# Performance work log

Hardware: AMD Instinct MI355X
Metric: run time of the kernel (lower is better)

## Reference

```python
import jax, jax.numpy as jnp
import numpy as np
from jax import lax

B, CIN, COUT, H, W, DG, K = 4, 128, 64, 128, 128, 16, 9
MAX_RES = 10.0  # max_residue_magnitude


def conv3x3(x, w, b):
    y = lax.conv_general_dilated(x, w, (1, 1), [(1, 1), (1, 1)],
                                 dimension_numbers=('NCHW', 'OIHW', 'NCHW'))
    return y + b[None, :, None, None]


def setup_inputs() -> dict:
    key = jax.random.key(0)
    ks = jax.random.split(key, 8)
    def rn(k, shape, s=0.05):
        return jax.random.normal(k, shape, jnp.float32) * s
    return {
        "x": jax.random.normal(ks[0], (B, CIN, H, W), jnp.float32),
        "extra_feat": jax.random.normal(ks[1], (B, 3 * COUT, H, W), jnp.float32),
        "w1": rn(ks[2], (COUT, 3 * COUT, 3, 3)), "b1": jnp.zeros((COUT,), jnp.float32),
        "w2": rn(ks[3], (COUT, COUT, 3, 3)), "b2": jnp.zeros((COUT,), jnp.float32),
        "w3": rn(ks[4], (COUT, COUT, 3, 3)), "b3": jnp.zeros((COUT,), jnp.float32),
        "w4": rn(ks[5], (27 * DG, COUT, 3, 3), 0.02), "b4": jnp.zeros((27 * DG,), jnp.float32),
        "weight": rn(ks[6], (COUT, CIN, 3, 3)), "bias": jnp.zeros((COUT,), jnp.float32),
    }


def deform_conv2d(x, offset, mask, weight, bias):
    # Modulated deformable conv, torchvision layout:
    # offset: [B, 2*DG*K, H, W] ordered (group, kernel_pos, (dy,dx))
    # mask:   [B, DG*K, H, W]
    Bn, Cin, Hh, Ww = x.shape
    Cg = Cin // DG
    off = offset.reshape(Bn, DG, K, 2, Hh, Ww)
    dy, dx = off[:, :, :, 0], off[:, :, :, 1]
    m = mask.reshape(Bn, DG, K, Hh, Ww)
    ki = (jnp.arange(K) // 3).reshape(1, 1, K, 1, 1).astype(x.dtype)
    kj = (jnp.arange(K) % 3).reshape(1, 1, K, 1, 1).astype(x.dtype)
    hh = jnp.arange(Hh, dtype=x.dtype).reshape(1, 1, 1, Hh, 1)
    ww = jnp.arange(Ww, dtype=x.dtype).reshape(1, 1, 1, 1, Ww)
    # sampling positions (stride=1, padding=1, dilation=1)
    py = hh - 1.0 + ki + dy  # [B,DG,K,H,W]
    px = ww - 1.0 + kj + dx
    y0 = jnp.floor(py)
    x0 = jnp.floor(px)
    ly = py - y0
    lx = px - x0
    xf = x.reshape(Bn, DG, Cg, Hh * Ww)

    def gather(yi, xi, wgt):
        valid = (yi >= 0) & (yi < Hh) & (xi >= 0) & (xi < Ww)
        yc = jnp.clip(yi, 0, Hh - 1).astype(jnp.int32)
        xc = jnp.clip(xi, 0, Ww - 1).astype(jnp.int32)
        idx = (yc * Ww + xc).reshape(Bn, DG, 1, K * Hh * Ww)
        g = jnp.take_along_axis(xf, jnp.broadcast_to(idx, (Bn, DG, Cg, K * Hh * Ww)), axis=3)
        g = g.reshape(Bn, DG, Cg, K, Hh, Ww)
        w_ = (wgt * valid.astype(x.dtype))[:, :, None]  # [B,DG,1,K,H,W]
        return g * w_

    val = (gather(y0, x0, (1 - ly) * (1 - lx))
           + gather(y0, x0 + 1, (1 - ly) * lx)
           + gather(y0 + 1, x0, ly * (1 - lx))
           + gather(y0 + 1, x0 + 1, ly * lx))
    val = val * m[:, :, None]  # modulation
    wk = weight.reshape(weight.shape[0], DG, Cg, K)
    out = jnp.einsum('bgckhw,ogck->bohw', val, wk) + bias[None, :, None, None]
    return out


def reference(x, extra_feat, w1, b1, w2, b2, w3, b3, w4, b4, weight, bias):
    lrelu = lambda t: jax.nn.leaky_relu(t, 0.1)
    t = lrelu(conv3x3(extra_feat, w1, b1))
    t = lrelu(conv3x3(t, w2, b2))
    t = lrelu(conv3x3(t, w3, b3))
    out = conv3x3(t, w4, b4)
    o1, o2, m = jnp.split(out, 3, axis=1)
    offset = MAX_RES * jnp.tanh(jnp.concatenate([o1, o2], axis=1))
    mask = jax.nn.sigmoid(m)
    return deform_conv2d(x, offset, mask, weight, bias)
```

## Files before the change

kernel.cpp:

```cpp
#include <hip/hip_runtime.h>
#include <cstdint>

#define H_ 128
#define W_ 128
#define HW 16384

typedef _Float16 f16x8 __attribute__((ext_vector_type(8)));
typedef _Float16 f16x4 __attribute__((ext_vector_type(4)));
typedef _Float16 f16x2 __attribute__((ext_vector_type(2)));
typedef float f32x4 __attribute__((ext_vector_type(4)));

__global__ __launch_bounds__(256)
void prep_all(const float* __restrict__ wd, const float* __restrict__ w1,
              const float* __restrict__ w2, const float* __restrict__ w3,
              const float* __restrict__ w4, const float* __restrict__ x,
              const float* __restrict__ ef,
              _Float16* __restrict__ wp, _Float16* __restrict__ A1,
              _Float16* __restrict__ A2, _Float16* __restrict__ A3,
              _Float16* __restrict__ A4, _Float16* __restrict__ xt,
              _Float16* __restrict__ ef_t) {
    __shared__ __align__(16) _Float16 t[128 * 200];
    const int bx  = blockIdx.x;
    const int tid = threadIdx.x;
    if (bx < 384) {
        int i = bx * 256 + tid;
        int kc = i % 96;
        int go = i / 96;
        int o = go & 63, g = go >> 6;
        float v = 0.f;
        if (kc < 72) { int k = kc >> 3, c = kc & 7; v = wd[(o * 128 + g * 8 + c) * 9 + k]; }
        wp[i] = (_Float16)v;
    } else if (bx < 2256) {
        const float* w; _Float16* Ap; int CIN, COUT, COpad, base;
        if (bx < 816)       { w = w1; Ap = A1; CIN = 192; COUT = 64;  COpad = 64;  base = 384; }
        else if (bx < 960)  { w = w2; Ap = A2; CIN = 64;  COUT = 64;  COpad = 64;  base = 816; }
        else if (bx < 1104) { w = w3; Ap = A3; CIN = 64;  COUT = 64;  COpad = 64;  base = 960; }
        else                { w = w4; Ap = A4; CIN = 64;  COUT = 432; COpad = 512; base = 1104; }
        int i = (bx - base) * 256 + tid;
        int kb = i / (COpad * 8);
        int rem = i - kb * (COpad * 8);
        int co = rem >> 3, j = rem & 7;
        int k = kb * 8 + j;
        int s = k / CIN;
        int ci = k - s * CIN;
        int kh = s / 3, kw = s % 3;
        float v = (co < COUT) ? w[((size_t)co * CIN + ci) * 9 + kh * 3 + kw] : 0.f;
        Ap[i] = (_Float16)v;
    } else if (bx < 6352) {
        int i = (bx - 2256) * 256 + tid;
        int px = i & 16383;
        int g  = (i >> 14) & 15;
        int b  = i >> 18;
        const float* xp = x + ((size_t)(b * 128 + g * 8) * HW) + px;
        f16x8 v;
        #pragma unroll
        for (int c = 0; c < 8; ++c) v[c] = (_Float16)xp[c * HW];
        *(f16x8*)(xt + (size_t)i * 8) = v;
    } else {
        int bb = bx - 6352;
        int b = bb >> 7, h = bb & 127;
        for (int i = tid; i < 192 * 128; i += 256) {
            int c = i >> 7, w = i & 127;
            t[w * 200 + c] = (_Float16)ef[((size_t)(b * 192 + c) * 128 + h) * 128 + w];
        }
        __syncthreads();
        _Float16* ob = ef_t + ((size_t)(b * 128 + h) * 128) * 192;
        for (int i = tid; i < 128 * 24; i += 256) {
            int px = i / 24, c8 = i % 24;
            *(f16x8*)(ob + px * 192 + c8 * 8) = *(const f16x8*)(t + px * 200 + c8 * 8);
        }
    }
}

template<int CIN_T, int COUT_T, int COpad_T, int NWM, int NWN, int MT, int NT,
         int ACT, int MINW>
__global__ __launch_bounds__(256, MINW)
void conv_mfma2(const _Float16* __restrict__ in, const _Float16* __restrict__ Ap,
                const float* __restrict__ bias, void* __restrict__ outp,
                _Float16* __restrict__ mskp) {
    constexpr int PX = 64;
    static_assert(NWM * NWN == 4 && NWN * NT * 16 == PX, "tiling");
    constexpr int TW  = PX + 2;
    constexpr int CPC = CIN_T / 8;
    constexpr int NKH = (CIN_T == 64) ? 3 : 1;
    constexpr int NST = 3 / NKH;
    constexpr int TC  = NKH * TW * CPC;
    constexpr int COg = NWM * MT * 16;
    __shared__ __align__(16) _Float16 lds[TC * 8];

    const int tid  = threadIdx.x;
    const int bxr  = (blockIdx.x & 7) * 128 + (blockIdx.x >> 3);
    const int ns   = bxr & 1;
    const int bh   = bxr >> 1;
    const int b    = bh >> 7;
    const int h    = bh & 127;
    const int cogB = blockIdx.y * COg;
    const int wv   = tid >> 6;
    const int wv_m = wv / NWN;
    const int wv_n = wv - wv_m * NWN;
    const int lane = tid & 63;
    const int quad = lane >> 4;
    const int l16  = lane & 15;
    const int w0g  = ns * PX;

    f32x4 acc[MT][NT];
    #pragma unroll
    for (int mt = 0; mt < MT; ++mt)
        #pragma unroll
        for (int nt = 0; nt < NT; ++nt) acc[mt][nt] = (f32x4){0.f, 0.f, 0.f, 0.f};

    const _Float16* inb = in + (size_t)b * (HW * CIN_T);

    auto stage = [&](int s) {
        for (int i = tid; i < TC; i += 256) {
            int kh_l = i / (TW * CPC);
            int r2   = i - kh_l * (TW * CPC);
            int wp_  = r2 / CPC;
            int c8   = r2 - wp_ * CPC;
            int kh   = s * NKH + kh_l;
            int hh   = h - 1 + kh;
            int w    = w0g + wp_ - 1;
            f16x8 v = (f16x8){0, 0, 0, 0, 0, 0, 0, 0};
            if ((unsigned)hh < 128u && (unsigned)w < 128u)
                v = *(const f16x8*)(inb + (hh * 128 + w) * CIN_T + c8 * 8);
            int slot = (c8 & ~7) | ((c8 & 7) ^ (wp_ & 7));
            ((f16x8*)lds)[(kh_l * TW + wp_) * CPC + slot] = v;
        }
    };

    auto compute = [&](int s) {
        #pragma unroll
        for (int kh_l = 0; kh_l < NKH; ++kh_l) {
            const int kh = s * NKH + kh_l;
            #pragma unroll
            for (int kwi = 0; kwi < 3; ++kwi) {
                #pragma unroll
                for (int ci32 = 0; ci32 < CIN_T / 32; ++ci32) {
                    const int kb0 = (kh * 3 + kwi) * CPC + ci32 * 4;
                    f16x8 aF[MT];
                    #pragma unroll
                    for (int mt = 0; mt < MT; ++mt) {
                        int co_m = cogB + (wv_m * MT + mt) * 16 + l16;
                        aF[mt] = *(const f16x8*)(Ap + ((size_t)(kb0 + quad) * COpad_T + co_m) * 8);
                    }
                    const int c8v = ci32 * 4 + quad;
                    #pragma unroll
                    for (int nt = 0; nt < NT; ++nt) {
                        int n  = (wv_n * NT + nt) * 16 + l16;
                        int wq = n + kwi;
                        int slot = (c8v & ~7) | ((c8v & 7) ^ (wq & 7));
                        f16x8 bF = ((const f16x8*)lds)[(kh_l * TW + wq) * CPC + slot];
                        #pragma unroll
                        for (int mt = 0; mt < MT; ++mt)
                            acc[mt][nt] = __builtin_amdgcn_mfma_f32_16x16x32_f16(aF[mt], bF, acc[mt][nt], 0, 0, 0);
                    }
                }
            }
        }
    };

    #pragma unroll 1
    for (int s = 0; s < NST; ++s) {
        __syncthreads();
        stage(s);
        __syncthreads();
        compute(s);
    }

    if constexpr (ACT == 1) {
        _Float16* ob = (_Float16*)outp + ((size_t)((b * 128 + h) * 128) + w0g) * 64;
        #pragma unroll
        for (int mt = 0; mt < MT; ++mt) {
            int co_b = (wv_m * MT + mt) * 16 + quad * 4;
            #pragma unroll
            for (int nt = 0; nt < NT; ++nt) {
                int px = (wv_n * NT + nt) * 16 + l16;
                f16x4 sv;
                #pragma unroll
                for (int r = 0; r < 4; ++r) {
                    float v = acc[mt][nt][r] + bias[co_b + r];
                    v = v > 0.f ? v : 0.1f * v;
                    sv[r] = (_Float16)v;
                }
                *(f16x4*)(ob + px * 64 + co_b) = sv;
            }
        }
    } else {
        _Float16* off2 = (_Float16*)outp;
        const int pxbase = h * 128 + w0g;
        #pragma unroll
        for (int mt = 0; mt < MT; ++mt) {
            int co_base = cogB + (wv_m * MT + mt) * 16 + quad * 4;
            #pragma unroll
            for (int r2 = 0; r2 < 2; ++r2) {
                int co0 = co_base + 2 * r2;
                if (co0 < 288) {
                    int g = co0 / 18;
                    int k = (co0 - g * 18) >> 1;
                    float bv0 = bias[co0], bv1 = bias[co0 + 1];
                    #pragma unroll
                    for (int nt = 0; nt < NT; ++nt) {
                        int px = (wv_n * NT + nt) * 16 + l16;
                        float v0 = acc[mt][nt][2 * r2]     + bv0;
                        float v1 = acc[mt][nt][2 * r2 + 1] + bv1;
                        float e0 = __expf(2.f * v0);
                        float e1 = __expf(2.f * v1);
                        f16x2 ov;
                        ov[0] = (_Float16)(10.f * (1.f - 2.f / (e0 + 1.f)));
                        ov[1] = (_Float16)(10.f * (1.f - 2.f / (e1 + 1.f)));
                        *(f16x2*)(off2 + (((size_t)(b * 16 + g) * 9 + k) * HW + pxbase + px) * 2) = ov;
                    }
                } else if (co0 < 432) {
                    #pragma unroll
                    for (int j = 0; j < 2; ++j) {
                        int co = co0 + j;
                        int mm = co - 288;
                        int g = mm / 9;
                        int k = mm - g * 9;
                        float bv = bias[co];
                        #pragma unroll
                        for (int nt = 0; nt < NT; ++nt) {
                            int px = (wv_n * NT + nt) * 16 + l16;
                            float v = acc[mt][nt][2 * r2 + j] + bv;
                            v = 1.f / (1.f + __expf(-v));
                            mskp[((size_t)(b * 16 + g) * 9 + k) * HW + pxbase + px] = (_Float16)v;
                        }
                    }
                }
            }
        }
    }
}

__global__ __launch_bounds__(256, 4)
void deform_fused(const _Float16* __restrict__ xt, const _Float16* __restrict__ off2,
                  const _Float16* __restrict__ msk, const _Float16* __restrict__ wp,
                  const float* __restrict__ bias, float* __restrict__ out) {
    __shared__ __align__(16) char vlds[2 * 64 * 256];
    const int tid  = threadIdx.x;
    const int bx   = (blockIdx.x & 7) * 128 + (blockIdx.x >> 3);
    const int ns   = bx & 1;
    const int bh   = bx >> 1;
    const int b    = bh >> 7;
    const int hrow = bh & 127;
    const int wv   = tid >> 6;
    const int lane = tid & 63;
    const int quad = lane >> 4;
    const int l16  = lane & 15;

    const int pxl   = tid & 63;
    const int kq    = tid >> 6;
    const int wglob = ns * 64 + pxl;
    const int pxg   = hrow * 128 + wglob;

    {
        f32x4 z = (f32x4){0.f, 0.f, 0.f, 0.f};
        for (int i = tid; i < 2048; i += 256) ((f32x4*)vlds)[i] = z;
    }
    __syncthreads();

    const _Float16* o2b = off2 + (size_t)b * 16 * 9 * HW * 2;
    const _Float16* mb  = msk  + (size_t)b * 16 * 9 * HW;

    f32x4 acc[4];
    #pragma unroll
    for (int nt = 0; nt < 4; ++nt) acc[nt] = (f32x4){0.f, 0.f, 0.f, 0.f};

    f16x2 od_c[3]; _Float16 m_c[3];
    #pragma unroll
    for (int i = 0; i < 3; ++i) {
        int k = kq + 4 * i;
        if (k < 9) {
            od_c[i] = *(const f16x2*)(o2b + ((size_t)(0 * 9 + k) * HW + pxg) * 2);
            m_c[i]  = mb[(size_t)(0 * 9 + k) * HW + pxg];
        }
    }

    #pragma unroll 1
    for (int gl = 0; gl < 16; ++gl) {
        const _Float16* xg = xt + ((size_t)(b * 16 + gl) * HW) * 8;
        char* vb = vlds + (gl & 1) * 16384;

        f16x8 aF[3];
        const _Float16* wg = wp + ((size_t)(gl * 64 + wv * 16 + l16)) * 96 + quad * 8;
        #pragma unroll
        for (int s = 0; s < 3; ++s) aF[s] = *(const f16x8*)(wg + s * 32);

        f16x2 od_n[3]; _Float16 m_n[3];
        if (gl < 15) {
            #pragma unroll
            for (int i = 0; i < 3; ++i) {
                int k = kq + 4 * i;
                if (k < 9) {
                    od_n[i] = *(const f16x2*)(o2b + ((size_t)((gl + 1) * 9 + k) * HW + pxg) * 2);
                    m_n[i]  = mb[(size_t)((gl + 1) * 9 + k) * HW + pxg];
                }
            }
        }

        #pragma unroll
        for (int i = 0; i < 3; ++i) {
            int k = kq + 4 * i;
            if (k < 9) {
                float dy = (float)od_c[i][0];
                float dx = (float)od_c[i][1];
                float m  = (float)m_c[i];
                float py  = (float)(hrow - 1 + k / 3) + dy;
                float pxf = (float)(wglob - 1 + k % 3) + dx;
                float y0f = floorf(py), x0f = floorf(pxf);
                float ly = py - y0f, lx = pxf - x0f;
                int y0 = (int)y0f, x0 = (int)x0f;
                int y1 = y0 + 1,  x1 = x0 + 1;
                float vy0 = ((unsigned)y0 < 128u) ? 1.f : 0.f;
                float vy1 = ((unsigned)y1 < 128u) ? 1.f : 0.f;
                float vx0 = ((unsigned)x0 < 128u) ? 1.f : 0.f;
                float vx1 = ((unsigned)x1 < 128u) ? 1.f : 0.f;
                float w00 = (1.f - ly) * (1.f - lx) * vy0 * vx0 * m;
                float w01 = (1.f - ly) * lx         * vy0 * vx1 * m;
                float w10 = ly * (1.f - lx)         * vy1 * vx0 * m;
                float w11 = ly * lx                 * vy1 * vx1 * m;
                int yc0 = min(max(y0, 0), 127), yc1 = min(max(y1, 0), 127);
                int xc0 = min(max(x0, 0), 127), xc1 = min(max(x1, 0), 127);
                f16x8 c00 = *(const f16x8*)(xg + (yc0 * W_ + xc0) * 8);
                f16x8 c01 = *(const f16x8*)(xg + (yc0 * W_ + xc1) * 8);
                f16x8 c10 = *(const f16x8*)(xg + (yc1 * W_ + xc0) * 8);
                f16x8 c11 = *(const f16x8*)(xg + (yc1 * W_ + xc1) * 8);
                _Float16 h00 = (_Float16)w00, h01 = (_Float16)w01;
                _Float16 h10 = (_Float16)w10, h11 = (_Float16)w11;
                f16x8 vv = c00 * h00 + c01 * h01 + c10 * h10 + c11 * h11;
                int chunk = k ^ (pxl & 15);
                *(f16x8*)(vb + pxl * 256 + chunk * 16) = vv;
            }
        }
        __syncthreads();

        #pragma unroll
        for (int nt = 0; nt < 4; ++nt) {
            int row = nt * 16 + l16;
            int sw  = row & 15;
            #pragma unroll
            for (int s = 0; s < 3; ++s) {
                f16x8 bF = *(const f16x8*)(vb + row * 256 + (((s << 2) + quad) ^ sw) * 16);
                acc[nt] = __builtin_amdgcn_mfma_f32_16x16x32_f16(aF[s], bF, acc[nt], 0, 0, 0);
            }
        }

        #pragma unroll
        for (int i = 0; i < 3; ++i) { od_c[i] = od_n[i]; m_c[i] = m_n[i]; }
    }

    __syncthreads();
    float* vf = (float*)vlds;
    #pragma unroll
    for (int r = 0; r < 4; ++r) {
        int o = wv * 16 + quad * 4 + r;
        #pragma unroll
        for (int nt = 0; nt < 4; ++nt) {
            int col = nt ^ quad;
            vf[o * 64 + col * 16 + l16] = acc[nt][r];
        }
    }
    __syncthreads();
    float* ob = out + ((size_t)(b * 64)) * HW + hrow * 128 + ns * 64;
    #pragma unroll
    for (int it = 0; it < 4; ++it) {
        int slot = tid + it * 256;
        int o    = slot >> 4;
        int p4   = slot & 15;
        int col  = (p4 >> 2) ^ ((o >> 2) & 3);
        f32x4 v = *(const f32x4*)(vf + o * 64 + col * 16 + (p4 & 3) * 4);
        float bv = bias[o];
        float4 sv = make_float4(v[0] + bv, v[1] + bv, v[2] + bv, v[3] + bv);
        *(float4*)(ob + (size_t)o * HW + p4 * 4) = sv;
    }
}

extern "C" void kernel_launch(void* const* d_in, const int* in_sizes, int n_in,
                              void* d_out, int out_size, void* d_ws, size_t ws_size,
                              hipStream_t stream) {
    const float* x  = (const float*)d_in[0];
    const float* ef = (const float*)d_in[1];
    const float* w1 = (const float*)d_in[2];
    const float* b1 = (const float*)d_in[3];
    const float* w2 = (const float*)d_in[4];
    const float* b2 = (const float*)d_in[5];
    const float* w3 = (const float*)d_in[6];
    const float* b3 = (const float*)d_in[7];
    const float* w4 = (const float*)d_in[8];
    const float* b4 = (const float*)d_in[9];
    const float* wd = (const float*)d_in[10];
    const float* bd = (const float*)d_in[11];
    float* out = (float*)d_out;

    char* ws = (char*)d_ws;
    _Float16* ef_t = (_Float16*)(ws);
    _Float16* tA   = (_Float16*)(ws + 25165824);
    _Float16* tB   = (_Float16*)(ws + 33554432);
    _Float16* off2 = (_Float16*)(ws + 41943040);
    _Float16* mskb = (_Float16*)(ws + 79691776);
    _Float16* wpd  = (_Float16*)(ws + 98566144);
    _Float16* A1   = (_Float16*)(ws + 98762752);
    _Float16* A2   = (_Float16*)(ws + 98983936);
    _Float16* A3   = (_Float16*)(ws + 99057664);
    _Float16* A4   = (_Float16*)(ws + 99131392);
    _Float16* xtb  = (_Float16*)(ws + 99721216);

    prep_all<<<6864, 256, 0, stream>>>(wd, w1, w2, w3, w4, x, ef,
                                       wpd, A1, A2, A3, A4, xtb, ef_t);

    conv_mfma2<192,  64,  64,  2,  2, 2, 2, 1, 4><<<dim3(1024, 1), 256, 0, stream>>>(ef_t, A1, b1, tA, nullptr);
    conv_mfma2< 64,  64,  64,  2,  2, 2, 2, 1, 4><<<dim3(1024, 1), 256, 0, stream>>>(tA, A2, b2, tB, nullptr);
    conv_mfma2< 64,  64,  64,  2,  2, 2, 2, 1, 4><<<dim3(1024, 1), 256, 0, stream>>>(tB, A3, b3, tA, nullptr);
    conv_mfma2< 64, 432, 512,  2,  2, 4, 2, 2, 2><<<dim3(1024, 4), 256, 0, stream>>>(tA, A4, b4, off2, mskb);

    deform_fused<<<1024, 256, 0, stream>>>(xtb, off2, mskb, wpd, bd, out);
}
```

Before: 315.0 us.

## Halve deform tile width to 32 pixels and double block count

```diff
diff --git a/kernel.cpp b/kernel.cpp
--- a/kernel.cpp
+++ b/kernel.cpp
@@ -236,11 +236,11 @@
 void deform_fused(const _Float16* __restrict__ xt, const _Float16* __restrict__ off2,
                   const _Float16* __restrict__ msk, const _Float16* __restrict__ wp,
                   const float* __restrict__ bias, float* __restrict__ out) {
-    __shared__ __align__(16) char vlds[2 * 64 * 256];
+    __shared__ __align__(16) char vlds[2 * 32 * 256];
     const int tid  = threadIdx.x;
-    const int bx   = (blockIdx.x & 7) * 128 + (blockIdx.x >> 3);
-    const int ns   = bx & 1;
-    const int bh   = bx >> 1;
+    const int bx   = (blockIdx.x & 7) * 256 + (blockIdx.x >> 3);
+    const int nq   = bx & 3;
+    const int bh   = bx >> 2;
     const int b    = bh >> 7;
     const int hrow = bh & 127;
     const int wv   = tid >> 6;
@@ -248,60 +248,59 @@
     const int quad = lane >> 4;
     const int l16  = lane & 15;
 
-    const int pxl   = tid & 63;
-    const int kq    = tid >> 6;
-    const int wglob = ns * 64 + pxl;
+    const int pxl   = tid & 31;
+    const int slot  = tid >> 5;
+    const int wglob = nq * 32 + pxl;
     const int pxg   = hrow * 128 + wglob;
+    const bool has2 = (slot == 0);
 
     {
         f32x4 z = (f32x4){0.f, 0.f, 0.f, 0.f};
-        for (int i = tid; i < 2048; i += 256) ((f32x4*)vlds)[i] = z;
+        for (int i = tid; i < 1024; i += 256) ((f32x4*)vlds)[i] = z;
     }
     __syncthreads();
 
     const _Float16* o2b = off2 + (size_t)b * 16 * 9 * HW * 2;
     const _Float16* mb  = msk  + (size_t)b * 16 * 9 * HW;
 
-    f32x4 acc[4];
-    #pragma unroll
-    for (int nt = 0; nt < 4; ++nt) acc[nt] = (f32x4){0.f, 0.f, 0.f, 0.f};
-
-    f16x2 od_c[3]; _Float16 m_c[3];
-    #pragma unroll
-    for (int i = 0; i < 3; ++i) {
-        int k = kq + 4 * i;
-        if (k < 9) {
-            od_c[i] = *(const f16x2*)(o2b + ((size_t)(0 * 9 + k) * HW + pxg) * 2);
-            m_c[i]  = mb[(size_t)(0 * 9 + k) * HW + pxg];
-        }
+    f32x4 acc[2];
+    acc[0] = (f32x4){0.f, 0.f, 0.f, 0.f};
+    acc[1] = (f32x4){0.f, 0.f, 0.f, 0.f};
+
+    f16x2 od_c[2]; _Float16 m_c[2];
+    od_c[0] = *(const f16x2*)(o2b + ((size_t)slot * HW + pxg) * 2);
+    m_c[0]  = mb[(size_t)slot * HW + pxg];
+    od_c[1] = od_c[0]; m_c[1] = m_c[0];
+    if (has2) {
+        od_c[1] = *(const f16x2*)(o2b + ((size_t)8 * HW + pxg) * 2);
+        m_c[1]  = mb[(size_t)8 * HW + pxg];
     }
 
     #pragma unroll 1
     for (int gl = 0; gl < 16; ++gl) {
         const _Float16* xg = xt + ((size_t)(b * 16 + gl) * HW) * 8;
-        char* vb = vlds + (gl & 1) * 16384;
+        char* vb = vlds + (gl & 1) * 8192;
 
         f16x8 aF[3];
         const _Float16* wg = wp + ((size_t)(gl * 64 + wv * 16 + l16)) * 96 + quad * 8;
         #pragma unroll
         for (int s = 0; s < 3; ++s) aF[s] = *(const f16x8*)(wg + s * 32);
 
-        f16x2 od_n[3]; _Float16 m_n[3];
+        f16x2 od_n[2]; _Float16 m_n[2];
+        od_n[0] = od_c[0]; od_n[1] = od_c[1]; m_n[0] = m_c[0]; m_n[1] = m_c[1];
         if (gl < 15) {
-            #pragma unroll
-            for (int i = 0; i < 3; ++i) {
-                int k = kq + 4 * i;
-                if (k < 9) {
-                    od_n[i] = *(const f16x2*)(o2b + ((size_t)((gl + 1) * 9 + k) * HW + pxg) * 2);
-                    m_n[i]  = mb[(size_t)((gl + 1) * 9 + k) * HW + pxg];
-                }
-            }
-        }
-
-        #pragma unroll
-        for (int i = 0; i < 3; ++i) {
-            int k = kq + 4 * i;
-            if (k < 9) {
+            od_n[0] = *(const f16x2*)(o2b + ((size_t)((gl + 1) * 9 + slot) * HW + pxg) * 2);
+            m_n[0]  = mb[(size_t)((gl + 1) * 9 + slot) * HW + pxg];
+            if (has2) {
+                od_n[1] = *(const f16x2*)(o2b + ((size_t)((gl + 1) * 9 + 8) * HW + pxg) * 2);
+                m_n[1]  = mb[(size_t)((gl + 1) * 9 + 8) * HW + pxg];
+            }
+        }
+
+        #pragma unroll
+        for (int i = 0; i < 2; ++i) {
+            if (i == 0 || has2) {
+                int k = (i == 0) ? slot : 8;
                 float dy = (float)od_c[i][0];
                 float dx = (float)od_c[i][1];
                 float m  = (float)m_c[i];
@@ -335,7 +334,7 @@
         __syncthreads();
 
         #pragma unroll
-        for (int nt = 0; nt < 4; ++nt) {
+        for (int nt = 0; nt < 2; ++nt) {
             int row = nt * 16 + l16;
             int sw  = row & 15;
             #pragma unroll
@@ -345,8 +344,7 @@
             }
         }
 
-        #pragma unroll
-        for (int i = 0; i < 3; ++i) { od_c[i] = od_n[i]; m_c[i] = m_n[i]; }
+        od_c[0] = od_n[0]; od_c[1] = od_n[1]; m_c[0] = m_n[0]; m_c[1] = m_n[1];
     }
 
     __syncthreads();
@@ -355,20 +353,20 @@
     for (int r = 0; r < 4; ++r) {
         int o = wv * 16 + quad * 4 + r;
         #pragma unroll
-        for (int nt = 0; nt < 4; ++nt) {
-            int col = nt ^ quad;
-            vf[o * 64 + col * 16 + l16] = acc[nt][r];
+        for (int nt = 0; nt < 2; ++nt) {
+            int col = nt ^ (quad & 1);
+            vf[o * 32 + col * 16 + l16] = acc[nt][r];
         }
     }
     __syncthreads();
-    float* ob = out + ((size_t)(b * 64)) * HW + hrow * 128 + ns * 64;
+    float* ob = out + ((size_t)(b * 64)) * HW + hrow * 128 + nq * 32;
     #pragma unroll
-    for (int it = 0; it < 4; ++it) {
-        int slot = tid + it * 256;
-        int o    = slot >> 4;
-        int p4   = slot & 15;
-        int col  = (p4 >> 2) ^ ((o >> 2) & 3);
-        f32x4 v = *(const f32x4*)(vf + o * 64 + col * 16 + (p4 & 3) * 4);
+    for (int it = 0; it < 2; ++it) {
+        int sl  = tid + it * 256;
+        int o   = sl >> 3;
+        int p4  = sl & 7;
+        int col = (p4 >> 2) ^ ((o >> 2) & 1);
+        f32x4 v = *(const f32x4*)(vf + o * 32 + col * 16 + (p4 & 3) * 4);
         float bv = bias[o];
         float4 sv = make_float4(v[0] + bv, v[1] + bv, v[2] + bv, v[3] + bv);
         *(float4*)(ob + (size_t)o * HW + p4 * 4) = sv;
@@ -413,5 +411,5 @@
     conv_mfma2< 64,  64,  64,  2,  2, 2, 2, 1, 4><<<dim3(1024, 1), 256, 0, stream>>>(tB, A3, b3, tA, nullptr);
     conv_mfma2< 64, 432, 512,  2,  2, 4, 2, 2, 2><<<dim3(1024, 4), 256, 0, stream>>>(tA, A4, b4, off2, mskb);
 
-    deform_fused<<<1024, 256, 0, stream>>>(xtb, off2, mskb, wpd, bd, out);
+    deform_fused<<<2048, 256, 0, stream>>>(xtb, off2, mskb, wpd, bd, out);
 }
```

Result: slower. 323.6 us (+2.7%).

## Software-pipeline deformable gathers one group ahead of MFMA compute

Applied to the files above, without the earlier changes.

```diff
diff --git a/kernel.cpp b/kernel.cpp
--- a/kernel.cpp
+++ b/kernel.cpp
@@ -266,45 +266,22 @@
     #pragma unroll
     for (int nt = 0; nt < 4; ++nt) acc[nt] = (f32x4){0.f, 0.f, 0.f, 0.f};
 
-    f16x2 od_c[3]; _Float16 m_c[3];
+    int ch[3];
     #pragma unroll
-    for (int i = 0; i < 3; ++i) {
-        int k = kq + 4 * i;
-        if (k < 9) {
-            od_c[i] = *(const f16x2*)(o2b + ((size_t)(0 * 9 + k) * HW + pxg) * 2);
-            m_c[i]  = mb[(size_t)(0 * 9 + k) * HW + pxg];
-        }
-    }
-
-    #pragma unroll 1
-    for (int gl = 0; gl < 16; ++gl) {
+    for (int i = 0; i < 3; ++i) ch[i] = (((kq + 4 * i) ^ (pxl & 15)) << 4);
+
+    f16x8 g00[3], g01[3], g10[3], g11[3];
+    _Float16 h00[3], h01[3], h10[3], h11[3];
+
+    auto issue = [&](int gl, const f16x2* od, const _Float16* m) {
         const _Float16* xg = xt + ((size_t)(b * 16 + gl) * HW) * 8;
-        char* vb = vlds + (gl & 1) * 16384;
-
-        f16x8 aF[3];
-        const _Float16* wg = wp + ((size_t)(gl * 64 + wv * 16 + l16)) * 96 + quad * 8;
-        #pragma unroll
-        for (int s = 0; s < 3; ++s) aF[s] = *(const f16x8*)(wg + s * 32);
-
-        f16x2 od_n[3]; _Float16 m_n[3];
-        if (gl < 15) {
-            #pragma unroll
-            for (int i = 0; i < 3; ++i) {
-                int k = kq + 4 * i;
-                if (k < 9) {
-                    od_n[i] = *(const f16x2*)(o2b + ((size_t)((gl + 1) * 9 + k) * HW + pxg) * 2);
-                    m_n[i]  = mb[(size_t)((gl + 1) * 9 + k) * HW + pxg];
-                }
-            }
-        }
-
         #pragma unroll
         for (int i = 0; i < 3; ++i) {
             int k = kq + 4 * i;
             if (k < 9) {
-                float dy = (float)od_c[i][0];
-                float dx = (float)od_c[i][1];
-                float m  = (float)m_c[i];
+                float dy = (float)od[i][0];
+                float dx = (float)od[i][1];
+                float mm = (float)m[i];
                 float py  = (float)(hrow - 1 + k / 3) + dy;
                 float pxf = (float)(wglob - 1 + k % 3) + dx;
                 float y0f = floorf(py), x0f = floorf(pxf);
@@ -315,25 +292,74 @@
                 float vy1 = ((unsigned)y1 < 128u) ? 1.f : 0.f;
                 float vx0 = ((unsigned)x0 < 128u) ? 1.f : 0.f;
                 float vx1 = ((unsigned)x1 < 128u) ? 1.f : 0.f;
-                float w00 = (1.f - ly) * (1.f - lx) * vy0 * vx0 * m;
-                float w01 = (1.f - ly) * lx         * vy0 * vx1 * m;
-                float w10 = ly * (1.f - lx)         * vy1 * vx0 * m;
-                float w11 = ly * lx                 * vy1 * vx1 * m;
+                h00[i] = (_Float16)((1.f - ly) * (1.f - lx) * vy0 * vx0 * mm);
+                h01[i] = (_Float16)((1.f - ly) * lx         * vy0 * vx1 * mm);
+                h10[i] = (_Float16)(ly * (1.f - lx)         * vy1 * vx0 * mm);
+                h11[i] = (_Float16)(ly * lx                 * vy1 * vx1 * mm);
                 int yc0 = min(max(y0, 0), 127), yc1 = min(max(y1, 0), 127);
                 int xc0 = min(max(x0, 0), 127), xc1 = min(max(x1, 0), 127);
-                f16x8 c00 = *(const f16x8*)(xg + (yc0 * W_ + xc0) * 8);
-                f16x8 c01 = *(const f16x8*)(xg + (yc0 * W_ + xc1) * 8);
-                f16x8 c10 = *(const f16x8*)(xg + (yc1 * W_ + xc0) * 8);
-                f16x8 c11 = *(const f16x8*)(xg + (yc1 * W_ + xc1) * 8);
-                _Float16 h00 = (_Float16)w00, h01 = (_Float16)w01;
-                _Float16 h10 = (_Float16)w10, h11 = (_Float16)w11;
-                f16x8 vv = c00 * h00 + c01 * h01 + c10 * h10 + c11 * h11;
-                int chunk = k ^ (pxl & 15);
-                *(f16x8*)(vb + pxl * 256 + chunk * 16) = vv;
-            }
-        }
+                g00[i] = *(const f16x8*)(xg + (yc0 * W_ + xc0) * 8);
+                g01[i] = *(const f16x8*)(xg + (yc0 * W_ + xc1) * 8);
+                g10[i] = *(const f16x8*)(xg + (yc1 * W_ + xc0) * 8);
+                g11[i] = *(const f16x8*)(xg + (yc1 * W_ + xc1) * 8);
+            }
+        }
+    };
+
+    auto finish = [&](int gl) {
+        char* vb = vlds + (gl & 1) * 16384;
+        #pragma unroll
+        for (int i = 0; i < 3; ++i) {
+            int k = kq + 4 * i;
+            if (k < 9) {
+                f16x8 vv = g00[i] * h00[i] + g01[i] * h01[i]
+                         + g10[i] * h10[i] + g11[i] * h11[i];
+                *(f16x8*)(vb + pxl * 256 + ch[i]) = vv;
+            }
+        }
+    };
+
+    {
+        f16x2 od0[3]; _Float16 m0[3];
+        #pragma unroll
+        for (int i = 0; i < 3; ++i) {
+            od0[i] = (f16x2){0, 0}; m0[i] = (_Float16)0.f;
+            int k = kq + 4 * i;
+            if (k < 9) {
+                od0[i] = *(const f16x2*)(o2b + ((size_t)k * HW + pxg) * 2);
+                m0[i]  = mb[(size_t)k * HW + pxg];
+            }
+        }
+        issue(0, od0, m0);
+    }
+
+    #pragma unroll 1
+    for (int gl = 0; gl < 16; ++gl) {
+        f16x2 od_n[3]; _Float16 m_n[3];
+        #pragma unroll
+        for (int i = 0; i < 3; ++i) { od_n[i] = (f16x2){0, 0}; m_n[i] = (_Float16)0.f; }
+        if (gl < 15) {
+            #pragma unroll
+            for (int i = 0; i < 3; ++i) {
+                int k = kq + 4 * i;
+                if (k < 9) {
+                    od_n[i] = *(const f16x2*)(o2b + ((size_t)((gl + 1) * 9 + k) * HW + pxg) * 2);
+                    m_n[i]  = mb[(size_t)((gl + 1) * 9 + k) * HW + pxg];
+                }
+            }
+        }
+
+        f16x8 aF[3];
+        const _Float16* wg = wp + ((size_t)(gl * 64 + wv * 16 + l16)) * 96 + quad * 8;
+        #pragma unroll
+        for (int s = 0; s < 3; ++s) aF[s] = *(const f16x8*)(wg + s * 32);
+
+        finish(gl);
         __syncthreads();
 
+        if (gl < 15) issue(gl + 1, od_n, m_n);
+
+        char* vb = vlds + (gl & 1) * 16384;
         #pragma unroll
         for (int nt = 0; nt < 4; ++nt) {
             int row = nt * 16 + l16;
@@ -344,9 +370,6 @@
                 acc[nt] = __builtin_amdgcn_mfma_f32_16x16x32_f16(aF[s], bF, acc[nt], 0, 0, 0);
             }
         }
-
-        #pragma unroll
-        for (int i = 0; i < 3; ++i) { od_c[i] = od_n[i]; m_c[i] = m_n[i]; }
     }
 
     __syncthreads();
```

New measurement: 316.7 us. About the same (+0.5%).

## Stage per-group input window in LDS for deformable bilinear gathers

Applied to the files above, without the earlier changes.

```diff
diff --git a/kernel.cpp b/kernel.cpp
--- a/kernel.cpp
+++ b/kernel.cpp
@@ -24,11 +24,17 @@
     const int tid = threadIdx.x;
     if (bx < 384) {
         int i = bx * 256 + tid;
-        int kc = i % 96;
-        int go = i / 96;
-        int o = go & 63, g = go >> 6;
+        int e = i & 7;
+        int chunk = i >> 3;
+        int o = chunk & 63;
+        int tq = chunk >> 6;
+        int q = tq & 3;
+        int u = tq >> 2;
+        int s = u % 3;
+        int g = u / 3;
+        int k = s * 4 + q;
         float v = 0.f;
-        if (kc < 72) { int k = kc >> 3, c = kc & 7; v = wd[(o * 128 + g * 8 + c) * 9 + k]; }
+        if (k < 9) v = wd[(o * 128 + g * 8 + e) * 9 + k];
         wp[i] = (_Float16)v;
     } else if (bx < 2256) {
         const float* w; _Float16* Ap; int CIN, COUT, COpad, base;
@@ -232,11 +238,15 @@
     }
 }
 
-__global__ __launch_bounds__(256, 4)
+__global__ __launch_bounds__(256, 3)
 void deform_fused(const _Float16* __restrict__ xt, const _Float16* __restrict__ off2,
                   const _Float16* __restrict__ msk, const _Float16* __restrict__ wp,
                   const float* __restrict__ bias, float* __restrict__ out) {
-    __shared__ __align__(16) char vlds[2 * 64 * 256];
+    constexpr int WROW = 24, WCOL = 89;
+    __shared__ __align__(16) char lds_all[WROW * WCOL * 16 + 64 * 256];
+    char* winb = lds_all;
+    char* vb   = lds_all + WROW * WCOL * 16;
+
     const int tid  = threadIdx.x;
     const int bx   = (blockIdx.x & 7) * 128 + (blockIdx.x >> 3);
     const int ns   = bx & 1;
@@ -252,12 +262,13 @@
     const int kq    = tid >> 6;
     const int wglob = ns * 64 + pxl;
     const int pxg   = hrow * 128 + wglob;
+    const int rbase = hrow - 11;
+    const int cbase = ns * 64 - 11;
 
     {
         f32x4 z = (f32x4){0.f, 0.f, 0.f, 0.f};
-        for (int i = tid; i < 2048; i += 256) ((f32x4*)vlds)[i] = z;
-    }
-    __syncthreads();
+        for (int i = tid; i < 1024; i += 256) ((f32x4*)vb)[i] = z;
+    }
 
     const _Float16* o2b = off2 + (size_t)b * 16 * 9 * HW * 2;
     const _Float16* mb  = msk  + (size_t)b * 16 * 9 * HW;
@@ -266,45 +277,29 @@
     #pragma unroll
     for (int nt = 0; nt < 4; ++nt) acc[nt] = (f32x4){0.f, 0.f, 0.f, 0.f};
 
-    f16x2 od_c[3]; _Float16 m_c[3];
-    #pragma unroll
-    for (int i = 0; i < 3; ++i) {
-        int k = kq + 4 * i;
-        if (k < 9) {
-            od_c[i] = *(const f16x2*)(o2b + ((size_t)(0 * 9 + k) * HW + pxg) * 2);
-            m_c[i]  = mb[(size_t)(0 * 9 + k) * HW + pxg];
-        }
-    }
-
-    #pragma unroll 1
-    for (int gl = 0; gl < 16; ++gl) {
+    auto stage_win = [&](int gl) {
         const _Float16* xg = xt + ((size_t)(b * 16 + gl) * HW) * 8;
-        char* vb = vlds + (gl & 1) * 16384;
-
-        f16x8 aF[3];
-        const _Float16* wg = wp + ((size_t)(gl * 64 + wv * 16 + l16)) * 96 + quad * 8;
-        #pragma unroll
-        for (int s = 0; s < 3; ++s) aF[s] = *(const f16x8*)(wg + s * 32);
-
-        f16x2 od_n[3]; _Float16 m_n[3];
-        if (gl < 15) {
-            #pragma unroll
-            for (int i = 0; i < 3; ++i) {
-                int k = kq + 4 * i;
-                if (k < 9) {
-                    od_n[i] = *(const f16x2*)(o2b + ((size_t)((gl + 1) * 9 + k) * HW + pxg) * 2);
-                    m_n[i]  = mb[(size_t)((gl + 1) * 9 + k) * HW + pxg];
-                }
-            }
-        }
-
+        #pragma unroll
+        for (int it = 0; it < 9; ++it) {
+            int i = tid + it * 256;
+            if (i < WROW * WCOL) {
+                int r = i / WCOL;
+                int c = i - r * WCOL;
+                int ry = min(max(rbase + r, 0), 127);
+                int cx = min(max(cbase + c, 0), 127);
+                *(f16x8*)(winb + i * 16) = *(const f16x8*)(xg + (ry * 128 + cx) * 8);
+            }
+        }
+    };
+
+    auto gather = [&](const f16x2* od, const _Float16* m) {
         #pragma unroll
         for (int i = 0; i < 3; ++i) {
             int k = kq + 4 * i;
             if (k < 9) {
-                float dy = (float)od_c[i][0];
-                float dx = (float)od_c[i][1];
-                float m  = (float)m_c[i];
+                float dy = (float)od[i][0];
+                float dx = (float)od[i][1];
+                float mm = (float)m[i];
                 float py  = (float)(hrow - 1 + k / 3) + dy;
                 float pxf = (float)(wglob - 1 + k % 3) + dx;
                 float y0f = floorf(py), x0f = floorf(pxf);
@@ -315,24 +310,59 @@
                 float vy1 = ((unsigned)y1 < 128u) ? 1.f : 0.f;
                 float vx0 = ((unsigned)x0 < 128u) ? 1.f : 0.f;
                 float vx1 = ((unsigned)x1 < 128u) ? 1.f : 0.f;
-                float w00 = (1.f - ly) * (1.f - lx) * vy0 * vx0 * m;
-                float w01 = (1.f - ly) * lx         * vy0 * vx1 * m;
-                float w10 = ly * (1.f - lx)         * vy1 * vx0 * m;
-                float w11 = ly * lx                 * vy1 * vx1 * m;
-                int yc0 = min(max(y0, 0), 127), yc1 = min(max(y1, 0), 127);
-                int xc0 = min(max(x0, 0), 127), xc1 = min(max(x1, 0), 127);
-                f16x8 c00 = *(const f16x8*)(xg + (yc0 * W_ + xc0) * 8);
-                f16x8 c01 = *(const f16x8*)(xg + (yc0 * W_ + xc1) * 8);
-                f16x8 c10 = *(const f16x8*)(xg + (yc1 * W_ + xc0) * 8);
-                f16x8 c11 = *(const f16x8*)(xg + (yc1 * W_ + xc1) * 8);
-                _Float16 h00 = (_Float16)w00, h01 = (_Float16)w01;
-                _Float16 h10 = (_Float16)w10, h11 = (_Float16)w11;
+                _Float16 h00 = (_Float16)((1.f - ly) * (1.f - lx) * vy0 * vx0 * mm);
+                _Float16 h01 = (_Float16)((1.f - ly) * lx         * vy0 * vx1 * mm);
+                _Float16 h10 = (_Float16)(ly * (1.f - lx)         * vy1 * vx0 * mm);
+                _Float16 h11 = (_Float16)(ly * lx                 * vy1 * vx1 * mm);
+                int ci = (y0 - rbase) * WCOL + (x0 - cbase);
+                f16x8 c00 = *(const f16x8*)(winb + ci * 16);
+                f16x8 c01 = *(const f16x8*)(winb + ci * 16 + 16);
+                f16x8 c10 = *(const f16x8*)(winb + (ci + WCOL) * 16);
+                f16x8 c11 = *(const f16x8*)(winb + (ci + WCOL) * 16 + 16);
                 f16x8 vv = c00 * h00 + c01 * h01 + c10 * h10 + c11 * h11;
-                int chunk = k ^ (pxl & 15);
-                *(f16x8*)(vb + pxl * 256 + chunk * 16) = vv;
-            }
-        }
+                *(f16x8*)(vb + pxl * 256 + ((k ^ (pxl & 15)) << 4)) = vv;
+            }
+        }
+    };
+
+    f16x2 od_c[3]; _Float16 m_c[3];
+    #pragma unroll
+    for (int i = 0; i < 3; ++i) {
+        od_c[i] = (f16x2){0, 0}; m_c[i] = (_Float16)0.f;
+        int k = kq + 4 * i;
+        if (k < 9) {
+            od_c[i] = *(const f16x2*)(o2b + ((size_t)k * HW + pxg) * 2);
+            m_c[i]  = mb[(size_t)k * HW + pxg];
+        }
+    }
+    stage_win(0);
+    __syncthreads();
+
+    #pragma unroll 1
+    for (int gl = 0; gl < 16; ++gl) {
+        f16x2 od_n[3]; _Float16 m_n[3];
+        #pragma unroll
+        for (int i = 0; i < 3; ++i) { od_n[i] = (f16x2){0, 0}; m_n[i] = (_Float16)0.f; }
+        if (gl < 15) {
+            #pragma unroll
+            for (int i = 0; i < 3; ++i) {
+                int k = kq + 4 * i;
+                if (k < 9) {
+                    od_n[i] = *(const f16x2*)(o2b + ((size_t)((gl + 1) * 9 + k) * HW + pxg) * 2);
+                    m_n[i]  = mb[(size_t)((gl + 1) * 9 + k) * HW + pxg];
+                }
+            }
+        }
+
+        gather(od_c, m_c);
         __syncthreads();
+
+        if (gl < 15) stage_win(gl + 1);
+
+        f16x8 aF[3];
+        #pragma unroll
+        for (int s = 0; s < 3; ++s)
+            aF[s] = *(const f16x8*)(wp + (size_t)((((gl * 3 + s) * 4 + quad) * 64) + wv * 16 + l16) * 8);
 
         #pragma unroll
         for (int nt = 0; nt < 4; ++nt) {
@@ -344,13 +374,13 @@
                 acc[nt] = __builtin_amdgcn_mfma_f32_16x16x32_f16(aF[s], bF, acc[nt], 0, 0, 0);
             }
         }
+        __syncthreads();
 
         #pragma unroll
         for (int i = 0; i < 3; ++i) { od_c[i] = od_n[i]; m_c[i] = m_n[i]; }
     }
 
-    __syncthreads();
-    float* vf = (float*)vlds;
+    float* vf = (float*)lds_all;
     #pragma unroll
     for (int r = 0; r < 4; ++r) {
         int o = wv * 16 + quad * 4 + r;
@@ -411,7 +441,7 @@
     conv_mfma2<192,  64,  64,  2,  2, 2, 2, 1, 4><<<dim3(1024, 1), 256, 0, stream>>>(ef_t, A1, b1, tA, nullptr);
     conv_mfma2< 64,  64,  64,  2,  2, 2, 2, 1, 4><<<dim3(1024, 1), 256, 0, stream>>>(tA, A2, b2, tB, nullptr);
     conv_mfma2< 64,  64,  64,  2,  2, 2, 2, 1, 4><<<dim3(1024, 1), 256, 0, stream>>>(tB, A3, b3, tA, nullptr);
-    conv_mfma2< 64, 432, 512,  2,  2, 4, 2, 2, 2><<<dim3(1024, 4), 256, 0, stream>>>(tA, A4, b4, off2, mskb);
+    conv_mfma2< 64, 432, 512,  4,  1, 4, 4, 2, 3><<<dim3(1024, 2), 256, 0, stream>>>(tA, A4, b4, off2, mskb);
 
     deform_fused<<<1024, 256, 0, stream>>>(xtb, off2, mskb, wpd, bd, out);
 }
```

New measurement: 335.3 us. 6.4% more time.
